# Kernel optimization log

Measured on AMD Instinct MI355X. Metric: run time of the kernel, lower is better.

## Reference

```python
import jax, jax.numpy as jnp
import numpy as np

B, N, C = 4, 4096, 256  # batch, num_points, channels (in=out=key)
LN_EPS = 1e-6
STAB = 1e-9


def setup_inputs() -> dict:
    key = jax.random.key(0)
    ks = jax.random.split(key, 12)
    s = 0.02
    return {
        "inputs": jax.random.normal(ks[0], (B, N, C), jnp.float32),
        "mask": jax.random.randint(ks[1], (B, N), 0, 2).astype(bool),
        "Wq": s * jax.random.normal(ks[2], (C, C), jnp.float32),
        "bq": jnp.zeros((C,), jnp.float32),
        "Wk": s * jax.random.normal(ks[3], (C, C), jnp.float32),
        "bk": jnp.zeros((C,), jnp.float32),
        "Wv": s * jax.random.normal(ks[4], (C, C), jnp.float32),
        "bv": jnp.zeros((C,), jnp.float32),
        "Wo": s * jax.random.normal(ks[5], (C, C), jnp.float32),
        "bo": jnp.zeros((C,), jnp.float32),
        "ln_scale": jnp.ones((C,), jnp.float32),
        "ln_bias": jnp.zeros((C,), jnp.float32),
    }


def reference(inputs, mask, Wq, bq, Wk, bk, Wv, bv, Wo, bo, ln_scale, ln_bias):
    # kernel_size=1 Conv == pointwise dense
    q = inputs @ Wq + bq  # [B,N,C]
    k = inputs @ Wk + bk
    v = inputs @ Wv + bv
    att = jnp.einsum('bmc,bnc->bmn', q, k)  # [B,M,N]
    attn_mask = mask[:, :, None] & mask[:, None, :]  # make_attention_mask then squeeze
    big_neg = jnp.finfo(att.dtype).min
    att = jnp.where(attn_mask, att, big_neg)
    att = jax.nn.softmax(att, axis=-1)
    # extra renormalization over the M (query) axis
    att = att / (STAB + jnp.sum(att, axis=1, keepdims=True))
    # NOTE: faithful to source einsum '...MN,...NC->...NC' (sums over M only)
    out = jnp.einsum('bmn,bnc->bnc', att, v)  # [B,N,C]
    out = out @ Wo + bo
    # LayerNorm with reduction_axes=-2 (normalize over points axis)
    mean = jnp.mean(out, axis=-2, keepdims=True)
    var = jnp.mean(jnp.square(out), axis=-2, keepdims=True) - jnp.square(mean)
    out = (out - mean) * jax.lax.rsqrt(var + LN_EPS) * ln_scale + ln_bias
    out = jax.nn.relu(out)
    return out + inputs
```

## Files before the change

### kernel.cpp

```cpp
#include <hip/hip_runtime.h>
#include <math.h>

#define BATCH 4
#define NPTS 4096
#define CH 256
#define LN_EPS 1e-6f

__global__ __launch_bounds__(256) void fuse_weights(
    const float* __restrict__ Wv, const float* __restrict__ bv,
    const float* __restrict__ Wo, const float* __restrict__ bo,
    float* __restrict__ Wc, float* __restrict__ bc) {
    const int j = threadIdx.x;
    const int i = blockIdx.x;
    if (i < CH) {
        float acc = 0.f;
        #pragma unroll 4
        for (int c = 0; c < CH; c += 4) {
            const float4 wv = *(const float4*)&Wv[i * CH + c];
            acc = fmaf(wv.x, Wo[(c + 0) * CH + j], acc);
            acc = fmaf(wv.y, Wo[(c + 1) * CH + j], acc);
            acc = fmaf(wv.z, Wo[(c + 2) * CH + j], acc);
            acc = fmaf(wv.w, Wo[(c + 3) * CH + j], acc);
        }
        Wc[i * CH + j] = acc;
    } else {
        float acc = bo[j];
        #pragma unroll 4
        for (int c = 0; c < CH; c += 4) {
            const float4 bv4 = *(const float4*)&bv[c];
            acc = fmaf(bv4.x, Wo[(c + 0) * CH + j], acc);
            acc = fmaf(bv4.y, Wo[(c + 1) * CH + j], acc);
            acc = fmaf(bv4.z, Wo[(c + 2) * CH + j], acc);
            acc = fmaf(bv4.w, Wo[(c + 3) * CH + j], acc);
        }
        bc[j] = acc;
    }
}

#define TM 64
#define TN 64
#define BK 32

__global__ __launch_bounds__(256) void gemm_u(
    const float* __restrict__ A, const float* __restrict__ Wc,
    const float* __restrict__ bc, float* __restrict__ u) {
    __shared__ float As[BK * TM];
    __shared__ float Bs[BK * TN];

    const int tid = threadIdx.x;
    const int m0 = blockIdx.x * TM;
    const int n0 = blockIdx.y * TN;
    const int tx = tid & 15;
    const int ty = tid >> 4;

    const int arow = tid >> 2;
    const int akq  = (tid & 3) * 8;
    const int brow = tid >> 3;
    const int bq   = (tid & 7) * 8;

    float acc[4][4] = {{0.f}};

    for (int kc = 0; kc < CH; kc += BK) {
        const float4 a0 = *(const float4*)&A[(size_t)(m0 + arow) * CH + kc + akq];
        const float4 a1 = *(const float4*)&A[(size_t)(m0 + arow) * CH + kc + akq + 4];
        const float4 b0 = *(const float4*)&Wc[(size_t)(kc + brow) * CH + n0 + bq];
        const float4 b1 = *(const float4*)&Wc[(size_t)(kc + brow) * CH + n0 + bq + 4];

        __syncthreads();
        As[(akq + 0) * TM + arow] = a0.x;
        As[(akq + 1) * TM + arow] = a0.y;
        As[(akq + 2) * TM + arow] = a0.z;
        As[(akq + 3) * TM + arow] = a0.w;
        As[(akq + 4) * TM + arow] = a1.x;
        As[(akq + 5) * TM + arow] = a1.y;
        As[(akq + 6) * TM + arow] = a1.z;
        As[(akq + 7) * TM + arow] = a1.w;
        *(float4*)&Bs[brow * TN + bq] = b0;
        *(float4*)&Bs[brow * TN + bq + 4] = b1;
        __syncthreads();

        #pragma unroll
        for (int k = 0; k < BK; ++k) {
            const float4 av = *(const float4*)&As[k * TM + ty * 4];
            const float4 bv4 = *(const float4*)&Bs[k * TN + tx * 4];
            const float am[4] = {av.x, av.y, av.z, av.w};
            const float bn[4] = {bv4.x, bv4.y, bv4.z, bv4.w};
            #pragma unroll
            for (int i = 0; i < 4; ++i)
                #pragma unroll
                for (int jj = 0; jj < 4; ++jj)
                    acc[i][jj] = fmaf(am[i], bn[jj], acc[i][jj]);
        }
    }

    const float4 bcv = *(const float4*)&bc[n0 + tx * 4];
    #pragma unroll
    for (int i = 0; i < 4; ++i) {
        float4 r;
        r.x = acc[i][0] + bcv.x;
        r.y = acc[i][1] + bcv.y;
        r.z = acc[i][2] + bcv.z;
        r.w = acc[i][3] + bcv.w;
        *(float4*)&u[(size_t)(m0 + ty * 4 + i) * CH + n0 + tx * 4] = r;
    }
}

__global__ __launch_bounds__(256) void ln_stats(
    const float* __restrict__ u, float* __restrict__ acc) {
    const int b = blockIdx.x;
    const int sl = blockIdx.y;
    const int c = threadIdx.x;
    const float* base = u + ((size_t)b * NPTS + (size_t)sl * 64) * CH + c;
    float s1 = 0.f, s2 = 0.f;
    #pragma unroll 8
    for (int n = 0; n < 64; ++n) {
        const float x = base[(size_t)n * CH];
        s1 += x;
        s2 = fmaf(x, x, s2);
    }
    atomicAdd(&acc[b * CH + c], s1);
    atomicAdd(&acc[BATCH * CH + b * CH + c], s2);
}

__global__ __launch_bounds__(256) void ln_finish(
    const float* __restrict__ u, const float* __restrict__ inp,
    const float* __restrict__ acc, const float* __restrict__ scale,
    const float* __restrict__ bias, float* __restrict__ out) {
    const int idx = blockIdx.x * blockDim.x + threadIdx.x;
    const int c4 = (idx & 63) * 4;
    const int bn = idx >> 6;
    const int b = bn >> 12;
    const size_t off = (size_t)idx * 4;

    const float4 uv = *(const float4*)&u[off];
    const float4 xv = *(const float4*)&inp[off];
    const float4 s1 = *(const float4*)&acc[b * CH + c4];
    const float4 s2 = *(const float4*)&acc[BATCH * CH + b * CH + c4];
    const float4 sc = *(const float4*)&scale[c4];
    const float4 bi = *(const float4*)&bias[c4];

    const float invN = 1.f / (float)NPTS;
    float uu[4] = {uv.x, uv.y, uv.z, uv.w};
    float xx[4] = {xv.x, xv.y, xv.z, xv.w};
    float a1[4] = {s1.x, s1.y, s1.z, s1.w};
    float a2[4] = {s2.x, s2.y, s2.z, s2.w};
    float scv[4] = {sc.x, sc.y, sc.z, sc.w};
    float biv[4] = {bi.x, bi.y, bi.z, bi.w};
    float r[4];
    #pragma unroll
    for (int j = 0; j < 4; ++j) {
        const float mean = a1[j] * invN;
        const float var = a2[j] * invN - mean * mean;
        const float inv = rsqrtf(var + LN_EPS);
        float y = (uu[j] - mean) * inv * scv[j] + biv[j];
        y = fmaxf(y, 0.f) + xx[j];
        r[j] = y;
    }
    float4 ro;
    ro.x = r[0]; ro.y = r[1]; ro.z = r[2]; ro.w = r[3];
    *(float4*)&out[off] = ro;
}

extern "C" void kernel_launch(void* const* d_in, const int* in_sizes, int n_in,
                              void* d_out, int out_size, void* d_ws, size_t ws_size,
                              hipStream_t stream) {
    const float* inputs   = (const float*)d_in[0];
    const float* Wv       = (const float*)d_in[6];
    const float* bv       = (const float*)d_in[7];
    const float* Wo       = (const float*)d_in[8];
    const float* bo       = (const float*)d_in[9];
    const float* ln_scale = (const float*)d_in[10];
    const float* ln_bias  = (const float*)d_in[11];
    float* out = (float*)d_out;

    float* Wc  = (float*)d_ws;
    float* bc  = Wc + CH * CH;
    float* u   = bc + CH;
    float* acc = u + (size_t)BATCH * NPTS * CH;

    hipMemsetAsync(acc, 0, 2 * BATCH * CH * sizeof(float), stream);
    fuse_weights<<<257, 256, 0, stream>>>(Wv, bv, Wo, bo, Wc, bc);
    gemm_u<<<dim3((BATCH * NPTS) / TM, CH / TN), 256, 0, stream>>>(inputs, Wc, bc, u);
    ln_stats<<<dim3(BATCH, 64), 256, 0, stream>>>(u, acc);
    ln_finish<<<(BATCH * NPTS * CH / 4) / 256, 256, 0, stream>>>(
        u, inputs, acc, ln_scale, ln_bias, out);
}
```

Baseline: 140.2 us.

## Use fp16 MFMA for fused GEMM and fold LayerNorm stats into epilogue

Replaces the fp32 SIMT GEMM with an fp16 MFMA 16x16x32 kernel. The combined weight matrix is precomputed in fp16, transposed, and kept fully in shared memory, while the fp32 activations are converted to fp16 as they are loaded. The per-channel sum and sum-of-squares for LayerNorm are now reduced in the GEMM epilogue with wave shuffles and atomics. This removes the separate ln_stats pass over u, and the zeroing of the accumulators moves into fuse_weights instead of a memset. The trade-off is reduced precision from fp16 operands and more atomic traffic per tile.

```diff
diff --git a/kernel.cpp b/kernel.cpp
--- a/kernel.cpp
+++ b/kernel.cpp
@@ -6,10 +6,14 @@
 #define CH 256
 #define LN_EPS 1e-6f
 
+typedef __attribute__((ext_vector_type(8))) _Float16 half8;
+typedef __attribute__((ext_vector_type(4))) float f32x4;
+
 __global__ __launch_bounds__(256) void fuse_weights(
     const float* __restrict__ Wv, const float* __restrict__ bv,
     const float* __restrict__ Wo, const float* __restrict__ bo,
-    float* __restrict__ Wc, float* __restrict__ bc) {
+    _Float16* __restrict__ Wct, float* __restrict__ bc,
+    float* __restrict__ accg) {
     const int j = threadIdx.x;
     const int i = blockIdx.x;
     if (i < CH) {
@@ -22,7 +26,7 @@
             acc = fmaf(wv.z, Wo[(c + 2) * CH + j], acc);
             acc = fmaf(wv.w, Wo[(c + 3) * CH + j], acc);
         }
-        Wc[i * CH + j] = acc;
+        Wct[(size_t)j * CH + i] = (_Float16)acc;
     } else {
         float acc = bo[j];
         #pragma unroll 4
@@ -34,97 +38,97 @@
             acc = fmaf(bv4.w, Wo[(c + 3) * CH + j], acc);
         }
         bc[j] = acc;
+        #pragma unroll
+        for (int t = 0; t < 2 * BATCH; ++t)
+            accg[t * CH + j] = 0.f;
     }
 }
 
-#define TM 64
-#define TN 64
-#define BK 32
+#define APAD 40
+#define BPAD 264
 
-__global__ __launch_bounds__(256) void gemm_u(
-    const float* __restrict__ A, const float* __restrict__ Wc,
-    const float* __restrict__ bc, float* __restrict__ u) {
-    __shared__ float As[BK * TM];
-    __shared__ float Bs[BK * TN];
+__global__ __launch_bounds__(256) void gemm_fused(
+    const float* __restrict__ A, const _Float16* __restrict__ Wct,
+    const float* __restrict__ bc, float* __restrict__ u,
+    float* __restrict__ accg) {
+    __shared__ _Float16 Bst[64][BPAD];
+    __shared__ _Float16 As[64][APAD];
 
     const int tid = threadIdx.x;
-    const int m0 = blockIdx.x * TM;
-    const int n0 = blockIdx.y * TN;
-    const int tx = tid & 15;
-    const int ty = tid >> 4;
+    const int m0 = blockIdx.x * 64;
+    const int n0 = blockIdx.y * 64;
+    const int w = tid >> 6;
+    const int l = tid & 63;
+    const int lr = l & 15;
+    const int lq = l >> 4;
 
-    const int arow = tid >> 2;
-    const int akq  = (tid & 3) * 8;
-    const int brow = tid >> 3;
-    const int bq   = (tid & 7) * 8;
-
-    float acc[4][4] = {{0.f}};
-
-    for (int kc = 0; kc < CH; kc += BK) {
-        const float4 a0 = *(const float4*)&A[(size_t)(m0 + arow) * CH + kc + akq];
-        const float4 a1 = *(const float4*)&A[(size_t)(m0 + arow) * CH + kc + akq + 4];
-        const float4 b0 = *(const float4*)&Wc[(size_t)(kc + brow) * CH + n0 + bq];
-        const float4 b1 = *(const float4*)&Wc[(size_t)(kc + brow) * CH + n0 + bq + 4];
-
-        __syncthreads();
-        As[(akq + 0) * TM + arow] = a0.x;
-        As[(akq + 1) * TM + arow] = a0.y;
-        As[(akq + 2) * TM + arow] = a0.z;
-        As[(akq + 3) * TM + arow] = a0.w;
-        As[(akq + 4) * TM + arow] = a1.x;
-        As[(akq + 5) * TM + arow] = a1.y;
-        As[(akq + 6) * TM + arow] = a1.z;
-        As[(akq + 7) * TM + arow] = a1.w;
-        *(float4*)&Bs[brow * TN + bq] = b0;
-        *(float4*)&Bs[brow * TN + bq + 4] = b1;
-        __syncthreads();
-
+    {
+        const int nr = tid >> 2;
+        const int ks = (tid & 3) * 64;
         #pragma unroll
-        for (int k = 0; k < BK; ++k) {
-            const float4 av = *(const float4*)&As[k * TM + ty * 4];
-            const float4 bv4 = *(const float4*)&Bs[k * TN + tx * 4];
-            const float am[4] = {av.x, av.y, av.z, av.w};
-            const float bn[4] = {bv4.x, bv4.y, bv4.z, bv4.w};
-            #pragma unroll
-            for (int i = 0; i < 4; ++i)
-                #pragma unroll
-                for (int jj = 0; jj < 4; ++jj)
-                    acc[i][jj] = fmaf(am[i], bn[jj], acc[i][jj]);
+        for (int i = 0; i < 8; ++i) {
+            half8 v = *(const half8*)&Wct[(size_t)(n0 + nr) * CH + ks + i * 8];
+            *(half8*)&Bst[nr][ks + i * 8] = v;
         }
     }
 
-    const float4 bcv = *(const float4*)&bc[n0 + tx * 4];
+    f32x4 acc[4];
     #pragma unroll
-    for (int i = 0; i < 4; ++i) {
-        float4 r;
-        r.x = acc[i][0] + bcv.x;
-        r.y = acc[i][1] + bcv.y;
-        r.z = acc[i][2] + bcv.z;
-        r.w = acc[i][3] + bcv.w;
-        *(float4*)&u[(size_t)(m0 + ty * 4 + i) * CH + n0 + tx * 4] = r;
+    for (int f = 0; f < 4; ++f) acc[f] = (f32x4){0.f, 0.f, 0.f, 0.f};
+
+    const int arow = tid >> 2;
+    const int akseg = (tid & 3) * 8;
+
+    for (int kc = 0; kc < CH; kc += 32) {
+        const float* aptr = &A[(size_t)(m0 + arow) * CH + kc + akseg];
+        const float4 a0 = *(const float4*)aptr;
+        const float4 a1 = *(const float4*)(aptr + 4);
+        half8 ah;
+        ah[0] = (_Float16)a0.x; ah[1] = (_Float16)a0.y;
+        ah[2] = (_Float16)a0.z; ah[3] = (_Float16)a0.w;
+        ah[4] = (_Float16)a1.x; ah[5] = (_Float16)a1.y;
+        ah[6] = (_Float16)a1.z; ah[7] = (_Float16)a1.w;
+
+        __syncthreads();
+        *(half8*)&As[arow][akseg] = ah;
+        __syncthreads();
+
+        const half8 afrag = *(const half8*)&As[w * 16 + lr][lq * 8];
+        #pragma unroll
+        for (int f = 0; f < 4; ++f) {
+            const half8 bfrag = *(const half8*)&Bst[f * 16 + lr][kc + lq * 8];
+            acc[f] = __builtin_amdgcn_mfma_f32_16x16x32_f16(afrag, bfrag, acc[f], 0, 0, 0);
+        }
     }
-}
 
-__global__ __launch_bounds__(256) void ln_stats(
-    const float* __restrict__ u, float* __restrict__ acc) {
-    const int b = blockIdx.x;
-    const int sl = blockIdx.y;
-    const int c = threadIdx.x;
-    const float* base = u + ((size_t)b * NPTS + (size_t)sl * 64) * CH + c;
-    float s1 = 0.f, s2 = 0.f;
-    #pragma unroll 8
-    for (int n = 0; n < 64; ++n) {
-        const float x = base[(size_t)n * CH];
-        s1 += x;
-        s2 = fmaf(x, x, s2);
+    const int batch = m0 >> 12;
+    const int mbase = m0 + w * 16 + lq * 4;
+    #pragma unroll
+    for (int f = 0; f < 4; ++f) {
+        const int n = n0 + f * 16 + lr;
+        const float bcn = bc[n];
+        float s1 = 0.f, s2 = 0.f;
+        #pragma unroll
+        for (int r = 0; r < 4; ++r) {
+            const float v = acc[f][r] + bcn;
+            u[(size_t)(mbase + r) * CH + n] = v;
+            s1 += v;
+            s2 = fmaf(v, v, s2);
+        }
+        s1 += __shfl_xor(s1, 16, 64);
+        s1 += __shfl_xor(s1, 32, 64);
+        s2 += __shfl_xor(s2, 16, 64);
+        s2 += __shfl_xor(s2, 32, 64);
+        if (lq == 0) {
+            atomicAdd(&accg[batch * CH + n], s1);
+            atomicAdd(&accg[BATCH * CH + batch * CH + n], s2);
+        }
     }
-    atomicAdd(&acc[b * CH + c], s1);
-    atomicAdd(&acc[BATCH * CH + b * CH + c], s2);
 }
 
 __global__ __launch_bounds__(256) void ln_finish(
     const float* __restrict__ u, const float* __restrict__ inp,
-    const float* __restrict__ acc, const float* __restrict__ scale,
+    const float* __restrict__ accg, const float* __restrict__ scale,
     const float* __restrict__ bias, float* __restrict__ out) {
     const int idx = blockIdx.x * blockDim.x + threadIdx.x;
     const int c4 = (idx & 63) * 4;
@@ -134,8 +138,8 @@
 
     const float4 uv = *(const float4*)&u[off];
     const float4 xv = *(const float4*)&inp[off];
-    const float4 s1 = *(const float4*)&acc[b * CH + c4];
-    const float4 s2 = *(const float4*)&acc[BATCH * CH + b * CH + c4];
+    const float4 s1 = *(const float4*)&accg[b * CH + c4];
+    const float4 s2 = *(const float4*)&accg[BATCH * CH + b * CH + c4];
     const float4 sc = *(const float4*)&scale[c4];
     const float4 bi = *(const float4*)&bias[c4];
 
@@ -153,8 +157,7 @@
         const float var = a2[j] * invN - mean * mean;
         const float inv = rsqrtf(var + LN_EPS);
         float y = (uu[j] - mean) * inv * scv[j] + biv[j];
-        y = fmaxf(y, 0.f) + xx[j];
-        r[j] = y;
+        r[j] = fmaxf(y, 0.f) + xx[j];
     }
     float4 ro;
     ro.x = r[0]; ro.y = r[1]; ro.z = r[2]; ro.w = r[3];
@@ -173,15 +176,14 @@
     const float* ln_bias  = (const float*)d_in[11];
     float* out = (float*)d_out;
 
-    float* Wc  = (float*)d_ws;
-    float* bc  = Wc + CH * CH;
-    float* u   = bc + CH;
-    float* acc = u + (size_t)BATCH * NPTS * CH;
+    float*     u    = (float*)d_ws;
+    float*     accg = (float*)((char*)d_ws + (size_t)BATCH * NPTS * CH * 4);
+    _Float16*  Wct  = (_Float16*)((char*)accg + 2 * BATCH * CH * 4);
+    float*     bc   = (float*)((char*)Wct + (size_t)CH * CH * 2);
 
-    hipMemsetAsync(acc, 0, 2 * BATCH * CH * sizeof(float), stream);
-    fuse_weights<<<257, 256, 0, stream>>>(Wv, bv, Wo, bo, Wc, bc);
-    gemm_u<<<dim3((BATCH * NPTS) / TM, CH / TN), 256, 0, stream>>>(inputs, Wc, bc, u);
-    ln_stats<<<dim3(BATCH, 64), 256, 0, stream>>>(u, acc);
+    fuse_weights<<<CH + 1, 256, 0, stream>>>(Wv, bv, Wo, bo, Wct, bc, accg);
+    gemm_fused<<<dim3((BATCH * NPTS) / 64, CH / 64), 256, 0, stream>>>(
+        inputs, Wct, bc, u, accg);
     ln_finish<<<(BATCH * NPTS * CH / 4) / 256, 256, 0, stream>>>(
-        u, inputs, acc, ln_scale, ln_bias, out);
+        u, inputs, accg, ln_scale, ln_bias, out);
 }
```

Result: faster. 121.6 us (-13.3%).
